# Kernel tuning notes

Measured on AMD Instinct MI355X. Metric: run time of the kernel, lower is better.

## Reference

```python
import jax, jax.numpy as jnp
import numpy as np

B, T, D = 512, 128, 512   # batch, encoder positions, input_size
H = 512                   # hidden_size
MID, BOT = 38, 38         # class counts


def setup_inputs() -> dict:
    key = jax.random.key(0)
    ks = jax.random.split(key, 12)
    s = lambda fan_in: 1.0 / np.sqrt(fan_in)
    inp = {
        "batch_H": jax.random.normal(ks[0], (B, T, D), dtype=jnp.float32),
        "mid_prev_text": jax.random.randint(ks[1], (B, 26), 0, MID, dtype=jnp.int64)
            if jax.config.jax_enable_x64 else jax.random.randint(ks[1], (B, 26), 0, MID).astype(jnp.int32),
        "bot_text": jax.random.randint(ks[2], (B, 26), 0, BOT).astype(jnp.int32),
        # AttentionCell params
        "W_i2h": jax.random.uniform(ks[3], (H, D), jnp.float32, -s(D), s(D)),
        "W_h2h": jax.random.uniform(ks[4], (H, H), jnp.float32, -s(H), s(H)),
        "b_h2h": jax.random.uniform(ks[5], (H,), jnp.float32, -s(H), s(H)),
        "W_score": jax.random.uniform(ks[6], (1, H), jnp.float32, -s(H), s(H)),
        # LSTMCell params: input dim = D + MID + BOT
        "W_ih": jax.random.uniform(ks[7], (4 * H, D + MID + BOT), jnp.float32, -s(H), s(H)),
        "W_hh": jax.random.uniform(ks[8], (4 * H, H), jnp.float32, -s(H), s(H)),
        "b_ih": jax.random.uniform(ks[9], (4 * H,), jnp.float32, -s(H), s(H)),
        "b_hh": jax.random.uniform(ks[10], (4 * H,), jnp.float32, -s(H), s(H)),
        # generator
        "W_gen": jax.random.uniform(ks[11], (MID, H), jnp.float32, -s(H), s(H)),
        "b_gen": jnp.zeros((MID,), jnp.float32),
        "batch_max_length": 25,
    }
    return inp


def reference(batch_H, mid_prev_text, bot_text, W_i2h, W_h2h, b_h2h, W_score,
              W_ih, W_hh, b_ih, b_hh, W_gen, b_gen, batch_max_length):
    num_steps = batch_max_length + 1
    bsz = batch_H.shape[0]
    hid = W_h2h.shape[0]

    # batch_H projection is step-independent: compute once. [B, T, H]
    batch_H_proj = jnp.einsum('btd,hd->bth', batch_H, W_i2h)

    # Precompute teacher-forced onehots, time-major: [num_steps, B, C]
    oh_mid = jax.nn.one_hot(mid_prev_text[:, :num_steps].T, MID, dtype=batch_H.dtype)
    oh_bot = jax.nn.one_hot(bot_text[:, :num_steps].T, BOT, dtype=batch_H.dtype)

    def step(carry, inputs):
        h, c = carry
        ohm, ohb = inputs
        # attention scores over T positions
        prev_proj = h @ W_h2h.T + b_h2h                       # [B, H]
        e = jnp.einsum('bth,oh->bto', jnp.tanh(batch_H_proj + prev_proj[:, None, :]), W_score)  # [B,T,1]
        alpha = jax.nn.softmax(e, axis=1)                     # [B, T, 1]
        context = jnp.einsum('bto,btd->bd', alpha, batch_H)   # [B, D]
        x = jnp.concatenate([context, ohm, ohb], axis=1)      # [B, D+MID+BOT]
        # LSTMCell (PyTorch gate order: i, f, g, o)
        gates = x @ W_ih.T + b_ih + h @ W_hh.T + b_hh         # [B, 4H]
        i_g, f_g, g_g, o_g = jnp.split(gates, 4, axis=1)
        i_g = jax.nn.sigmoid(i_g)
        f_g = jax.nn.sigmoid(f_g)
        g_g = jnp.tanh(g_g)
        o_g = jax.nn.sigmoid(o_g)
        c_new = f_g * c + i_g * g_g
        h_new = o_g * jnp.tanh(c_new)
        return (h_new, c_new), h_new

    h0 = jnp.zeros((bsz, hid), batch_H.dtype)
    c0 = jnp.zeros((bsz, hid), batch_H.dtype)
    (_, _), hiddens = jax.lax.scan(step, (h0, c0), (oh_mid, oh_bot))  # [S, B, H]
    output_hiddens = jnp.transpose(hiddens, (1, 0, 2))                 # [B, S, H]
    g = jnp.einsum('bsh,ch->bsc', output_hiddens, W_gen) + b_gen       # [B, S, MID]
    return g
```

## Files before the change

### kernel.cpp

```cpp
#include <hip/hip_runtime.h>
#include <hip/hip_bf16.h>
#include <hip/hip_fp16.h>
#include <cstdint>
#include <cstddef>

#define B_   512
#define T_   128
#define D_   512
#define H_   512
#define MID_ 38
#define BOT_ 38
#define S_   26
#define XL_  588

typedef unsigned short u16;
typedef __attribute__((ext_vector_type(8))) short bf16x8v;
typedef __attribute__((ext_vector_type(8))) _Float16 f16x8v;
typedef __attribute__((ext_vector_type(8))) unsigned short u16x8;
typedef __attribute__((ext_vector_type(4))) float f32x4v;

__device__ __forceinline__ u16 f2bf_rn(float f){
  unsigned u = __float_as_uint(f);
  return (u16)((u + 0x7fffu + ((u>>16)&1u)) >> 16);
}
__device__ __forceinline__ float bf2f(u16 v){ return __uint_as_float(((unsigned)v)<<16); }
__device__ __forceinline__ u16 f2h_u(float f){ return __half_as_ushort(__float2half(f)); }
__device__ __forceinline__ float h2f_u(u16 u){ return __half2float(__ushort_as_half(u)); }

__device__ __forceinline__ float fast_tanh(float x){
  return 1.0f - 2.0f*__builtin_amdgcn_rcpf(__expf(2.0f*x) + 1.0f);
}
__device__ __forceinline__ float fast_sig(float x){
  return __builtin_amdgcn_rcpf(1.0f + __expf(-x));
}

__device__ __forceinline__ void cvt_hilo4(const float* src, u16* hi, u16* lo){
  float4 v = *(const float4*)src;
  ushort4 h, l;
  h.x=f2bf_rn(v.x); h.y=f2bf_rn(v.y); h.z=f2bf_rn(v.z); h.w=f2bf_rn(v.w);
  l.x=f2bf_rn(v.x-bf2f(h.x)); l.y=f2bf_rn(v.y-bf2f(h.y));
  l.z=f2bf_rn(v.z-bf2f(h.z)); l.w=f2bf_rn(v.w-bf2f(h.w));
  *(ushort4*)hi = h; *(ushort4*)lo = l;
}

__global__ __launch_bounds__(256) void setup_all(
    const float* __restrict__ bH,
    const float* __restrict__ Wi2h, const float* __restrict__ Wh2h,
    const float* __restrict__ Whh,  const float* __restrict__ Wih,
    const float* __restrict__ Wgen, const float* __restrict__ bh2h,
    const float* __restrict__ bih,  const float* __restrict__ bhh,
    u16* __restrict__ bHh,
    u16* __restrict__ Wi2h_h, u16* __restrict__ Bh2_hi, u16* __restrict__ Bh2_lo,
    u16* __restrict__ Bih_hi, u16* __restrict__ Bih_lo,
    u16* __restrict__ Wg_hi,  u16* __restrict__ Wg_lo,
    float* __restrict__ WmT, float* __restrict__ WbT, float* __restrict__ bcombF,
    u16* __restrict__ hA_hi, u16* __restrict__ hA_lo, float* __restrict__ c)
{
  const int T0 = 8388608;
  const int T1 = T0+65536;
  const int T2 = T1+65536;
  const int T3 = T2+262144;
  const int T4 = T3+262144;
  const int T5 = T4+8192;
  const int T6 = T5+19456;
  const int T7 = T6+640;
  const int T8 = T7+65536;
  const int T9 = T8+65536;
  for (int i = blockIdx.x*256 + threadIdx.x; i < T9; i += gridDim.x*256){
    if (i < T0){
      int row=i>>7, c4=(i&127)*4;
      float4 v = *(const float4*)&bH[(size_t)row*512 + c4];
      ushort4 h; h.x=f2h_u(v.x); h.y=f2h_u(v.y); h.z=f2h_u(v.z); h.w=f2h_u(v.w);
      *(ushort4*)&bHh[(size_t)row*512 + c4] = h;
    } else if (i < T1){
      int j=i-T0, row=j>>7, c4=(j&127)*4;
      float4 v = *(const float4*)&Wi2h[(size_t)row*512 + c4];
      ushort4 h; h.x=f2h_u(v.x); h.y=f2h_u(v.y); h.z=f2h_u(v.z); h.w=f2h_u(v.w);
      *(ushort4*)&Wi2h_h[(size_t)row*512 + c4] = h;
    } else if (i < T2){
      int j=i-T1, row=j>>7, c4=(j&127)*4;
      cvt_hilo4(&Wh2h[(size_t)row*512+c4], &Bh2_hi[(size_t)row*512+c4], &Bh2_lo[(size_t)row*512+c4]);
    } else if (i < T3){
      int j=i-T2, row=j>>7, c4=(j&127)*4;
      cvt_hilo4(&Whh[(size_t)row*512+c4],
                &Bh2_hi[(size_t)(512+row)*512+c4], &Bh2_lo[(size_t)(512+row)*512+c4]);
    } else if (i < T4){
      int j=i-T3, row=j>>7, c4=(j&127)*4;
      cvt_hilo4(&Wih[(size_t)row*XL_+c4], &Bih_hi[(size_t)row*512+c4], &Bih_lo[(size_t)row*512+c4]);
    } else if (i < T5){
      int j=i-T4, row=j>>7, c4=(j&127)*4;
      float4 v = make_float4(0.f,0.f,0.f,0.f);
      if (row < MID_) v = *(const float4*)&Wgen[(size_t)row*512 + c4];
      ushort4 h, l;
      h.x=f2bf_rn(v.x); h.y=f2bf_rn(v.y); h.z=f2bf_rn(v.z); h.w=f2bf_rn(v.w);
      l.x=f2bf_rn(v.x-bf2f(h.x)); l.y=f2bf_rn(v.y-bf2f(h.y));
      l.z=f2bf_rn(v.z-bf2f(h.z)); l.w=f2bf_rn(v.w-bf2f(h.w));
      *(ushort4*)&Wg_hi[(size_t)row*512+c4] = h;
      *(ushort4*)&Wg_lo[(size_t)row*512+c4] = l;
    } else if (i < T6){
      int j=i-T5;
      int cc=j>>9, jq=j&511;
#pragma unroll
      for (int u=0;u<4;u++){
        int jj=jq*4+u;
        WmT[(size_t)cc*2048+jj] = Wih[(size_t)jj*XL_ + 512 + cc];
        WbT[(size_t)cc*2048+jj] = Wih[(size_t)jj*XL_ + 512 + MID_ + cc];
      }
    } else if (i < T7){
      int j=(i-T6)*4;
#pragma unroll
      for (int u=0;u<4;u++){
        int k=j+u;
        if (k < 512) bcombF[k] = bh2h[k];
        else if (k < 2560) bcombF[k] = bih[k-512] + bhh[k-512];
      }
    } else if (i < T8){
      int j=i-T7;
      ushort4 z = {0,0,0,0};
      *(ushort4*)&hA_hi[(size_t)j*4] = z;
      *(ushort4*)&hA_lo[(size_t)j*4] = z;
    } else {
      int j=i-T8;
      *(float4*)&c[(size_t)j*4] = make_float4(0.f,0.f,0.f,0.f);
    }
  }
}

__global__ __launch_bounds__(256) void gemm_proj16(
    const u16* __restrict__ Ah, const u16* __restrict__ Bh,
    u16* __restrict__ projh)
{
  extern __shared__ char smem[];
  constexpr int STR = 40;
  short* As = (short*)smem;
  short* Bs = As + 128*STR;
  const int tid=threadIdx.x;
  const int n = blockIdx.x;
  const int x = n & 7, q = n >> 3;
  const int bn = (q & 3) * 128;
  const int bm = ((q >> 2)*8 + x) * 128;
  const int w=tid>>6, lane=tid&63, wr=w>>1, wc=w&1;

  f32x4v acc[4][4];
#pragma unroll
  for (int i=0;i<4;i++)
#pragma unroll
    for (int j=0;j<4;j++) acc[i][j] = (f32x4v){0.f,0.f,0.f,0.f};

  u16x8 ra[2], rb[2];
  auto load = [&](int it){
    const int kk = it<<5;
#pragma unroll
    for (int L=0; L<2; L++){
      int t=L*256+tid, row=t>>2, c=(t&3)*8;
      ra[L] = *(const u16x8*)&Ah[(size_t)(bm+row)*512 + kk + c];
      rb[L] = *(const u16x8*)&Bh[(size_t)(bn+row)*512 + kk + c];
    }
  };
  load(0);

  for (int it=0; it<16; ++it){
    __syncthreads();
#pragma unroll
    for (int L=0; L<2; L++){
      int t=L*256+tid, row=t>>2, c=(t&3)*8;
      *(u16x8*)&As[row*STR+c] = ra[L];
      *(u16x8*)&Bs[row*STR+c] = rb[L];
    }
    if (it+1 < 16) load(it+1);
    __syncthreads();
    const int koff = (lane>>4)*8, mrow = lane&15;
#pragma unroll
    for (int i=0;i<4;i++)
#pragma unroll
      for (int j=0;j<4;j++){
        f16x8v af = *(const f16x8v*)&As[(wr*64+i*16+mrow)*STR + koff];
        f16x8v bf = *(const f16x8v*)&Bs[(wc*64+j*16+mrow)*STR + koff];
        acc[i][j] = __builtin_amdgcn_mfma_f32_16x16x32_f16(af, bf, acc[i][j], 0,0,0);
      }
  }

  const int r0 = (lane>>4)*4, cn = lane&15;
  __syncthreads();
  u16* Ts = (u16*)smem;
#pragma unroll
  for (int i=0;i<4;i++)
#pragma unroll
    for (int j=0;j<4;j++)
#pragma unroll
      for (int r=0;r<4;r++)
        Ts[(wr*64+i*16+r0+r)*128 + wc*64+j*16+cn] = f2h_u(acc[i][j][r]);
  __syncthreads();
#pragma unroll
  for (int q2=0;q2<8;q2++){
    int idx = q2*256 + tid;
    int row = idx>>4, c8 = (idx&15)*8;
    *(float4*)&projh[(size_t)(bm+row)*512 + bn + c8] = *(const float4*)&Ts[row*128 + c8];
  }
}

template<int BM,int BN,int MODE>
__global__ __launch_bounds__(256) void gemm_bf(
    const u16* __restrict__ Ah, const u16* __restrict__ Al, int lda,
    const u16* __restrict__ Bh, const u16* __restrict__ Bl, int ldb,
    float* __restrict__ Cout, int ldc,
    const float* __restrict__ bias2, int npass, int kSteps)
{
  extern __shared__ char smem[];
  constexpr int STR = 40;
  short* As = (short*)smem;
  short* Bs = As + BM*STR;
  const int tid=threadIdx.x, bm=blockIdx.y*BM, bn=blockIdx.x*BN;
  const int w=tid>>6, lane=tid&63, wr=w>>1, wc=w&1;
  constexpr int WM=BM/2, WN=BN/2, FM=WM/16, FN=WN/16;
  constexpr int LA=BM/64, LB=BN/64;
  const int nIter = npass*kSteps;

  f32x4v acc[FM][FN];
#pragma unroll
  for (int i=0;i<FM;i++)
#pragma unroll
    for (int j=0;j<FN;j++) acc[i][j] = (f32x4v){0.f,0.f,0.f,0.f};

  u16x8 ra[LA], rb[LB];
  auto load = [&](int it){
    const int pass = it/kSteps, kk = (it%kSteps)<<5;
    const u16* Ap = (pass==2)?Al:Ah;
    const u16* Bp = (pass==1)?Bl:Bh;
#pragma unroll
    for (int L=0; L<LA; L++){
      int t=L*256+tid, row=t>>2, c=(t&3)*8;
      ra[L] = *(const u16x8*)&Ap[(size_t)(bm+row)*lda + kk + c];
    }
#pragma unroll
    for (int L=0; L<LB; L++){
      int t=L*256+tid, row=t>>2, c=(t&3)*8;
      rb[L] = *(const u16x8*)&Bp[(size_t)(bn+row)*ldb + kk + c];
    }
  };
  load(0);

  for (int it=0; it<nIter; ++it){
    __syncthreads();
#pragma unroll
    for (int L=0; L<LA; L++){ int t=L*256+tid; *(u16x8*)&As[(t>>2)*STR+(t&3)*8] = ra[L]; }
#pragma unroll
    for (int L=0; L<LB; L++){ int t=L*256+tid; *(u16x8*)&Bs[(t>>2)*STR+(t&3)*8] = rb[L]; }
    if (it+1 < nIter) load(it+1);
    __syncthreads();
    const int koff = (lane>>4)*8, mrow = lane&15;
#pragma unroll
    for (int i=0;i<FM;i++)
#pragma unroll
      for (int j=0;j<FN;j++){
        bf16x8v af = *(const bf16x8v*)&As[(wr*WM+i*16+mrow)*STR + koff];
        bf16x8v bf = *(const bf16x8v*)&Bs[(wc*WN+j*16+mrow)*STR + koff];
        acc[i][j] = __builtin_amdgcn_mfma_f32_16x16x32_bf16(af, bf, acc[i][j], 0,0,0);
      }
  }

  const int r0 = (lane>>4)*4, cn = lane&15;
  if constexpr (MODE==2){
#pragma unroll
    for (int i=0;i<FM;i++)
#pragma unroll
      for (int j=0;j<FN;j++)
#pragma unroll
        for (int r=0;r<4;r++){
          int m = bm + wr*WM + i*16 + r0 + r;
          int n2 = bn + wc*WN + j*16 + cn;
          if (n2 < MID_){
            int s = m >> 9, b = m & 511;
            Cout[((size_t)b*S_ + s)*MID_ + n2] = acc[i][j][r] + bias2[n2];
          }
        }
  } else {
#pragma unroll
    for (int i=0;i<FM;i++)
#pragma unroll
      for (int j=0;j<FN;j++)
#pragma unroll
        for (int r=0;r<4;r++){
          int row = bm + wr*WM + i*16 + r0 + r;
          int col = bn + wc*WN + j*16 + cn;
          float v = acc[i][j][r];
          if (bias2) v += bias2[col];
          Cout[(size_t)row*ldc + col] = v;
        }
  }
}

__global__ __launch_bounds__(1024) void attn_kernel(
    const u16* __restrict__ projh, const float* __restrict__ combo,
    const float* __restrict__ Wscore, const u16* __restrict__ bHh,
    u16* __restrict__ ctx_hi, u16* __restrict__ ctx_lo)
{
  __shared__ float s_e[T_];
  __shared__ float s_red[32];
  __shared__ float s_part[16][D_];
  const int tid=threadIdx.x, b=blockIdx.x, wave=tid>>6, lane=tid&63;

  float pv[8], wv[8];
  {
    const float* pprow = combo + (size_t)b*2560;
    float4 p0=*(const float4*)&pprow[lane*8], p1=*(const float4*)&pprow[lane*8+4];
    float4 w0=*(const float4*)&Wscore[lane*8], w1=*(const float4*)&Wscore[lane*8+4];
    pv[0]=p0.x;pv[1]=p0.y;pv[2]=p0.z;pv[3]=p0.w;pv[4]=p1.x;pv[5]=p1.y;pv[6]=p1.z;pv[7]=p1.w;
    wv[0]=w0.x;wv[1]=w0.y;wv[2]=w0.z;wv[3]=w0.w;wv[4]=w1.x;wv[5]=w1.y;wv[6]=w1.z;wv[7]=w1.w;
  }
  {
    const u16* base = projh + (size_t)b*T_*H_ + lane*8;
    u16x8 cur = *(const u16x8*)(base + (size_t)wave*H_);
    for (int t=wave; t<T_; t+=16){
      u16x8 nxt;
      if (t+16 < T_) nxt = *(const u16x8*)(base + (size_t)(t+16)*H_);
      float acc = 0.f;
#pragma unroll
      for (int j=0;j<8;j++) acc += wv[j]*fast_tanh(h2f_u(cur[j]) + pv[j]);
#pragma unroll
      for (int o=32;o>0;o>>=1) acc += __shfl_down(acc,o);
      if (lane==0) s_e[t] = acc;
      cur = nxt;
    }
  }
  __syncthreads();
  float v = (tid < T_) ? s_e[tid] : -INFINITY;
  float m = v;
#pragma unroll
  for (int o=32;o>0;o>>=1) m = fmaxf(m, __shfl_down(m,o));
  if (tid < T_ && lane==0) s_red[wave] = m;
  __syncthreads();
  m = fmaxf(s_red[0], s_red[1]);
  float p = (tid < T_) ? __expf(v - m) : 0.f;
  float sum = p;
#pragma unroll
  for (int o=32;o>0;o>>=1) sum += __shfl_down(sum,o);
  if (tid < T_ && lane==0) s_red[16+wave] = sum;
  __syncthreads();
  float denom = s_red[16] + s_red[17];
  if (tid < T_) s_e[tid] = p/denom;
  __syncthreads();

  const int d0 = lane*8;
  float a[8] = {0,0,0,0,0,0,0,0};
  {
    const u16* base = bHh + (size_t)b*T_*D_ + d0;
    u16x8 cur = *(const u16x8*)(base + (size_t)(wave*8)*D_);
    for (int t=wave*8; t<wave*8+8; ++t){
      u16x8 nxt;
      if (t+1 < wave*8+8) nxt = *(const u16x8*)(base + (size_t)(t+1)*D_);
      const float al = s_e[t];
#pragma unroll
      for (int j=0;j<8;j++) a[j] += al*h2f_u(cur[j]);
      cur = nxt;
    }
  }
  *(float4*)&s_part[wave][d0]   = make_float4(a[0],a[1],a[2],a[3]);
  *(float4*)&s_part[wave][d0+4] = make_float4(a[4],a[5],a[6],a[7]);
  __syncthreads();
  if (tid < D_){
    float vv = s_part[0][tid];
#pragma unroll
    for (int q=1;q<16;q++) vv += s_part[q][tid];
    u16 hh=f2bf_rn(vv), ll=f2bf_rn(vv-bf2f(hh));
    ctx_hi[(size_t)b*512 + tid] = hh;
    ctx_lo[(size_t)b*512 + tid] = ll;
  }
}

__global__ __launch_bounds__(256) void gates_lstm(
    const u16* __restrict__ Ah, const u16* __restrict__ Al,
    const u16* __restrict__ Bh, const u16* __restrict__ Bl,
    const float* __restrict__ combo,
    const float* __restrict__ WmT, const float* __restrict__ WbT,
    const int* __restrict__ midtok, const int* __restrict__ bottok,
    float* __restrict__ c,
    u16* __restrict__ hA_hi, u16* __restrict__ hA_lo,
    u16* __restrict__ hid_hi, u16* __restrict__ hid_lo, int s)
{
  constexpr int STR = 72;
  __shared__ short Bs[64*STR];
  const int tid=threadIdx.x, lane=tid&63, w=tid>>6;
  const int j0 = blockIdx.x*16, bm = blockIdx.y*64;
  const int mrow=lane&15, koff=(lane>>4)*8;
  const int arow = bm + w*16 + mrow;
  const int srow = tid>>2, scc=(tid&3)*8;
  const int sbrow = (srow>>4)*512 + j0 + (srow&15);

  f32x4v acc[4];
#pragma unroll
  for (int f=0;f<4;f++) acc[f] = (f32x4v){0.f,0.f,0.f,0.f};

  u16x8 sb0, sb1;
  bf16x8v a0[2], a1[2];
  auto loadB = [&](int it){
    const int pass = it>>3, kk=(it&7)<<6;
    const u16* Bp = (pass==1)?Bl:Bh;
    sb0 = *(const u16x8*)&Bp[(size_t)sbrow*512 + kk + scc];
    sb1 = *(const u16x8*)&Bp[(size_t)sbrow*512 + kk + scc + 32];
  };
  auto loadA0 = [&](int it){
    const int pass = it>>3, kk=(it&7)<<6;
    const u16* Ap = (pass==2)?Al:Ah;
    a0[0] = *(const bf16x8v*)&Ap[(size_t)arow*512 + kk + koff];
    a0[1] = *(const bf16x8v*)&Ap[(size_t)arow*512 + kk + koff + 32];
  };
  auto loadA1 = [&](int it){
    const int pass = it>>3, kk=(it&7)<<6;
    const u16* Ap = (pass==2)?Al:Ah;
    a1[0] = *(const bf16x8v*)&Ap[(size_t)arow*512 + kk + koff];
    a1[1] = *(const bf16x8v*)&Ap[(size_t)arow*512 + kk + koff + 32];
  };

  loadB(0); loadA0(0);
  for (int it=0; it<24; it+=2){
    __syncthreads();
    *(u16x8*)&Bs[srow*STR+scc]    = sb0;
    *(u16x8*)&Bs[srow*STR+scc+32] = sb1;
    if (it+1 < 24){ loadB(it+1); loadA1(it+1); }
    __syncthreads();
#pragma unroll
    for (int f=0;f<4;f++){
      bf16x8v b0 = *(const bf16x8v*)&Bs[(f*16+mrow)*STR + koff];
      bf16x8v b1 = *(const bf16x8v*)&Bs[(f*16+mrow)*STR + koff + 32];
      acc[f] = __builtin_amdgcn_mfma_f32_16x16x32_bf16(a0[0], b0, acc[f], 0,0,0);
      acc[f] = __builtin_amdgcn_mfma_f32_16x16x32_bf16(a0[1], b1, acc[f], 0,0,0);
    }
    if (it+1 >= 24) break;
    __syncthreads();
    *(u16x8*)&Bs[srow*STR+scc]    = sb0;
    *(u16x8*)&Bs[srow*STR+scc+32] = sb1;
    if (it+2 < 24){ loadB(it+2); loadA0(it+2); }
    __syncthreads();
#pragma unroll
    for (int f=0;f<4;f++){
      bf16x8v b0 = *(const bf16x8v*)&Bs[(f*16+mrow)*STR + koff];
      bf16x8v b1 = *(const bf16x8v*)&Bs[(f*16+mrow)*STR + koff + 32];
      acc[f] = __builtin_amdgcn_mfma_f32_16x16x32_bf16(a1[0], b0, acc[f], 0,0,0);
      acc[f] = __builtin_amdgcn_mfma_f32_16x16x32_bf16(a1[1], b1, acc[f], 0,0,0);
    }
  }

  const int r0=(lane>>4)*4, jj=lane&15, j=j0+jj;
#pragma unroll
  for (int r=0;r<4;r++){
    const int b = bm + w*16 + r0 + r;
    const int mt = midtok[b*26 + s];
    const int bt = bottok[b*26 + s];
    const float* wm = WmT + (size_t)mt*2048;
    const float* wb = WbT + (size_t)bt*2048;
    const float* cb = combo + (size_t)b*2560 + 512;
    float ig = acc[0][r] + cb[j       ] + wm[j       ] + wb[j       ];
    float fg = acc[1][r] + cb[512 + j ] + wm[512 + j ] + wb[512 + j ];
    float gg = acc[2][r] + cb[1024 + j] + wm[1024 + j] + wb[1024 + j];
    float og = acc[3][r] + cb[1536 + j] + wm[1536 + j] + wb[1536 + j];
    ig = fast_sig(ig);
    fg = fast_sig(fg);
    gg = fast_tanh(gg);
    og = fast_sig(og);
    const size_t ci = (size_t)b*512 + j;
    const float cn = fg*c[ci] + ig*gg;
    const float hn = og*fast_tanh(cn);
    c[ci] = cn;
    u16 hh = f2bf_rn(hn), hl = f2bf_rn(hn - bf2f(hh));
    hA_hi[ci] = hh;
    hA_lo[ci] = hl;
    hid_hi[((size_t)s*512 + b)*512 + j] = hh;
    hid_lo[((size_t)s*512 + b)*512 + j] = hl;
  }
}

extern "C" void kernel_launch(void* const* d_in, const int* in_sizes, int n_in,
                              void* d_out, int out_size, void* d_ws, size_t ws_size,
                              hipStream_t stream) {
  const float* bH   = (const float*)d_in[0];
  const int*   midt = (const int*)  d_in[1];
  const int*   bott = (const int*)  d_in[2];
  const float* Wi2h = (const float*)d_in[3];
  const float* Wh2h = (const float*)d_in[4];
  const float* bh2h = (const float*)d_in[5];
  const float* Wsc  = (const float*)d_in[6];
  const float* Wih  = (const float*)d_in[7];
  const float* Whh  = (const float*)d_in[8];
  const float* bih  = (const float*)d_in[9];
  const float* bhh  = (const float*)d_in[10];
  const float* Wgen = (const float*)d_in[11];
  const float* bgen = (const float*)d_in[12];
  float* out = (float*)d_out;

  char* wp = (char*)d_ws;
  u16* projh   = (u16*)wp; wp += (size_t)B_*T_*H_*2;
  u16* bHh     = (u16*)wp; wp += (size_t)B_*T_*D_*2;
  u16* Bh2_hi  = (u16*)wp; wp += (size_t)2560*512*2;
  u16* Bh2_lo  = (u16*)wp; wp += (size_t)2560*512*2;
  u16* Bih_hi  = (u16*)wp; wp += (size_t)2048*512*2;
  u16* Bih_lo  = (u16*)wp; wp += (size_t)2048*512*2;
  u16* Wi2h_h  = (u16*)wp; wp += (size_t)512*512*2;
  u16* Wg_hi   = (u16*)wp; wp += (size_t)64*512*2;
  u16* Wg_lo   = (u16*)wp; wp += (size_t)64*512*2;
  u16* ctx_hi  = (u16*)wp; wp += (size_t)B_*512*2;
  u16* ctx_lo  = (u16*)wp; wp += (size_t)B_*512*2;
  u16* hA_hi   = (u16*)wp; wp += (size_t)B_*512*2;
  u16* hA_lo   = (u16*)wp; wp += (size_t)B_*512*2;
  u16* hid_hi  = (u16*)wp; wp += (size_t)S_*B_*H_*2;
  u16* hid_lo  = (u16*)wp; wp += (size_t)S_*B_*H_*2;
  float* combo = (float*)wp; wp += (size_t)B_*2560*4;
  float* c     = (float*)wp; wp += (size_t)B_*H_*4;
  float* bcombF= (float*)wp; wp += (size_t)2560*4;
  float* WmT   = (float*)wp; wp += (size_t)MID_*2048*4;
  float* WbT   = (float*)wp; wp += (size_t)BOT_*2048*4;
  if ((size_t)(wp - (char*)d_ws) > ws_size) return;

  setup_all<<<4096, 256, 0, stream>>>(
      bH, Wi2h, Wh2h, Whh, Wih, Wgen, bh2h, bih, bhh,
      bHh, Wi2h_h, Bh2_hi, Bh2_lo, Bih_hi, Bih_lo, Wg_hi, Wg_lo,
      WmT, WbT, bcombF, hA_hi, hA_lo, c);

  gemm_proj16<<<2048, 256, 32768, stream>>>(bHh, Wi2h_h, projh);

  for (int s=0; s<S_; ++s){
    gemm_bf<64,64,0><<<dim3(40,8), 256, 10240, stream>>>(
        hA_hi, hA_lo, 512, Bh2_hi, Bh2_lo, 512,
        combo, 2560, bcombF, 3, 16);
    attn_kernel<<<B_, 1024, 0, stream>>>(
        projh, combo, Wsc, bHh, ctx_hi, ctx_lo);
    gates_lstm<<<dim3(32,8), 256, 0, stream>>>(
        ctx_hi, ctx_lo, Bih_hi, Bih_lo, combo, WmT, WbT,
        midt, bott, c, hA_hi, hA_lo,
        hid_hi, hid_lo, s);
  }

  gemm_bf<64,64,2><<<dim3(1,208), 256, 10240, stream>>>(
      hid_hi, hid_lo, 512, Wg_hi, Wg_lo, 512,
      out, 0, bgen, 3, 16);
}
```

Before: 1.655 ms.

## Use direct global-to-LDS loads in GEMMs and streamline attention softmax

Both GEMM kernels now use global_load_lds to copy tiles straight into shared memory. This replaces the register-staged double-buffer prefetch and the padded stride of 40 with an unpadded stride of 32, and the shared-memory launch sizes shrink to match. The attention kernel prefetches the first context rows before the score loop and does the softmax in one wavefront with xor shuffles, which removes two block barriers. In exchange, loads no longer overlap compute across K iterations, and the unpadded LDS layout may cause bank conflicts on the MFMA fragment reads.

Result: slower. 1.817 ms (+9.8%).

```diff
diff --git a/kernel.cpp b/kernel.cpp
--- a/kernel.cpp
+++ b/kernel.cpp
@@ -32,6 +32,12 @@
 }
 __device__ __forceinline__ float fast_sig(float x){
   return __builtin_amdgcn_rcpf(1.0f + __expf(-x));
+}
+
+typedef __attribute__((address_space(1))) const unsigned gu32;
+typedef __attribute__((address_space(3))) unsigned lu32;
+__device__ __forceinline__ void gload16(const void* g, void* l){
+  __builtin_amdgcn_global_load_lds((gu32*)g, (lu32*)l, 16, 0, 0);
 }
 
 __device__ __forceinline__ void cvt_hilo4(const float* src, u16* hi, u16* lo){
@@ -131,9 +137,8 @@
     u16* __restrict__ projh)
 {
   extern __shared__ char smem[];
-  constexpr int STR = 40;
   short* As = (short*)smem;
-  short* Bs = As + 128*STR;
+  short* Bs = As + 128*32;
   const int tid=threadIdx.x;
   const int n = blockIdx.x;
   const int x = n & 7, q = n >> 3;
@@ -147,41 +152,28 @@
 #pragma unroll
     for (int j=0;j<4;j++) acc[i][j] = (f32x4v){0.f,0.f,0.f,0.f};
 
-  u16x8 ra[2], rb[2];
-  auto load = [&](int it){
+  for (int it=0; it<16; ++it){
     const int kk = it<<5;
 #pragma unroll
     for (int L=0; L<2; L++){
       int t=L*256+tid, row=t>>2, c=(t&3)*8;
-      ra[L] = *(const u16x8*)&Ah[(size_t)(bm+row)*512 + kk + c];
-      rb[L] = *(const u16x8*)&Bh[(size_t)(bn+row)*512 + kk + c];
-    }
-  };
-  load(0);
-
-  for (int it=0; it<16; ++it){
-    __syncthreads();
-#pragma unroll
-    for (int L=0; L<2; L++){
-      int t=L*256+tid, row=t>>2, c=(t&3)*8;
-      *(u16x8*)&As[row*STR+c] = ra[L];
-      *(u16x8*)&Bs[row*STR+c] = rb[L];
-    }
-    if (it+1 < 16) load(it+1);
+      gload16(&Ah[(size_t)(bm+row)*512 + kk + c], &As[t*8]);
+      gload16(&Bh[(size_t)(bn+row)*512 + kk + c], &Bs[t*8]);
+    }
     __syncthreads();
     const int koff = (lane>>4)*8, mrow = lane&15;
 #pragma unroll
     for (int i=0;i<4;i++)
 #pragma unroll
       for (int j=0;j<4;j++){
-        f16x8v af = *(const f16x8v*)&As[(wr*64+i*16+mrow)*STR + koff];
-        f16x8v bf = *(const f16x8v*)&Bs[(wc*64+j*16+mrow)*STR + koff];
+        f16x8v af = *(const f16x8v*)&As[(wr*64+i*16+mrow)*32 + koff];
+        f16x8v bf = *(const f16x8v*)&Bs[(wc*64+j*16+mrow)*32 + koff];
         acc[i][j] = __builtin_amdgcn_mfma_f32_16x16x32_f16(af, bf, acc[i][j], 0,0,0);
       }
+    __syncthreads();
   }
 
   const int r0 = (lane>>4)*4, cn = lane&15;
-  __syncthreads();
   u16* Ts = (u16*)smem;
 #pragma unroll
   for (int i=0;i<4;i++)
@@ -207,9 +199,8 @@
     const float* __restrict__ bias2, int npass, int kSteps)
 {
   extern __shared__ char smem[];
-  constexpr int STR = 40;
   short* As = (short*)smem;
-  short* Bs = As + BM*STR;
+  short* Bs = As + BM*32;
   const int tid=threadIdx.x, bm=blockIdx.y*BM, bn=blockIdx.x*BN;
   const int w=tid>>6, lane=tid&63, wr=w>>1, wc=w&1;
   constexpr int WM=BM/2, WN=BN/2, FM=WM/16, FN=WN/16;
@@ -222,41 +213,31 @@
 #pragma unroll
     for (int j=0;j<FN;j++) acc[i][j] = (f32x4v){0.f,0.f,0.f,0.f};
 
-  u16x8 ra[LA], rb[LB];
-  auto load = [&](int it){
+  for (int it=0; it<nIter; ++it){
     const int pass = it/kSteps, kk = (it%kSteps)<<5;
     const u16* Ap = (pass==2)?Al:Ah;
     const u16* Bp = (pass==1)?Bl:Bh;
 #pragma unroll
     for (int L=0; L<LA; L++){
       int t=L*256+tid, row=t>>2, c=(t&3)*8;
-      ra[L] = *(const u16x8*)&Ap[(size_t)(bm+row)*lda + kk + c];
+      gload16(&Ap[(size_t)(bm+row)*lda + kk + c], &As[t*8]);
     }
 #pragma unroll
     for (int L=0; L<LB; L++){
       int t=L*256+tid, row=t>>2, c=(t&3)*8;
-      rb[L] = *(const u16x8*)&Bp[(size_t)(bn+row)*ldb + kk + c];
-    }
-  };
-  load(0);
-
-  for (int it=0; it<nIter; ++it){
-    __syncthreads();
-#pragma unroll
-    for (int L=0; L<LA; L++){ int t=L*256+tid; *(u16x8*)&As[(t>>2)*STR+(t&3)*8] = ra[L]; }
-#pragma unroll
-    for (int L=0; L<LB; L++){ int t=L*256+tid; *(u16x8*)&Bs[(t>>2)*STR+(t&3)*8] = rb[L]; }
-    if (it+1 < nIter) load(it+1);
+      gload16(&Bp[(size_t)(bn+row)*ldb + kk + c], &Bs[t*8]);
+    }
     __syncthreads();
     const int koff = (lane>>4)*8, mrow = lane&15;
 #pragma unroll
     for (int i=0;i<FM;i++)
 #pragma unroll
       for (int j=0;j<FN;j++){
-        bf16x8v af = *(const bf16x8v*)&As[(wr*WM+i*16+mrow)*STR + koff];
-        bf16x8v bf = *(const bf16x8v*)&Bs[(wc*WN+j*16+mrow)*STR + koff];
+        bf16x8v af = *(const bf16x8v*)&As[(wr*WM+i*16+mrow)*32 + koff];
+        bf16x8v bf = *(const bf16x8v*)&Bs[(wc*WN+j*16+mrow)*32 + koff];
         acc[i][j] = __builtin_amdgcn_mfma_f32_16x16x32_bf16(af, bf, acc[i][j], 0,0,0);
       }
+    __syncthreads();
   }
 
   const int r0 = (lane>>4)*4, cn = lane&15;
@@ -296,9 +277,10 @@
     u16* __restrict__ ctx_hi, u16* __restrict__ ctx_lo)
 {
   __shared__ float s_e[T_];
-  __shared__ float s_red[32];
   __shared__ float s_part[16][D_];
   const int tid=threadIdx.x, b=blockIdx.x, wave=tid>>6, lane=tid&63;
+  const int d0 = lane*8;
+  const u16* cbase = bHh + (size_t)b*T_*D_ + d0;
 
   float pv[8], wv[8];
   {
@@ -308,6 +290,10 @@
     pv[0]=p0.x;pv[1]=p0.y;pv[2]=p0.z;pv[3]=p0.w;pv[4]=p1.x;pv[5]=p1.y;pv[6]=p1.z;pv[7]=p1.w;
     wv[0]=w0.x;wv[1]=w0.y;wv[2]=w0.z;wv[3]=w0.w;wv[4]=w1.x;wv[5]=w1.y;wv[6]=w1.z;wv[7]=w1.w;
   }
+  u16x8 pf[4];
+#pragma unroll
+  for (int r=0;r<4;r++) pf[r] = *(const u16x8*)(cbase + (size_t)(wave*8+r)*D_);
+
   {
     const u16* base = projh + (size_t)b*T_*H_ + lane*8;
     u16x8 cur = *(const u16x8*)(base + (size_t)wave*H_);
@@ -324,36 +310,36 @@
     }
   }
   __syncthreads();
-  float v = (tid < T_) ? s_e[tid] : -INFINITY;
-  float m = v;
-#pragma unroll
-  for (int o=32;o>0;o>>=1) m = fmaxf(m, __shfl_down(m,o));
-  if (tid < T_ && lane==0) s_red[wave] = m;
+  if (wave==0){
+    float v0 = s_e[lane], v1 = s_e[lane+64];
+    float mm = fmaxf(v0, v1);
+#pragma unroll
+    for (int o=32;o>0;o>>=1) mm = fmaxf(mm, __shfl_xor(mm,o));
+    float p0 = __expf(v0-mm), p1 = __expf(v1-mm);
+    float ss = p0 + p1;
+#pragma unroll
+    for (int o=32;o>0;o>>=1) ss += __shfl_xor(ss,o);
+    const float inv = __builtin_amdgcn_rcpf(ss);
+    s_e[lane]    = p0*inv;
+    s_e[lane+64] = p1*inv;
+  }
   __syncthreads();
-  m = fmaxf(s_red[0], s_red[1]);
-  float p = (tid < T_) ? __expf(v - m) : 0.f;
-  float sum = p;
-#pragma unroll
-  for (int o=32;o>0;o>>=1) sum += __shfl_down(sum,o);
-  if (tid < T_ && lane==0) s_red[16+wave] = sum;
-  __syncthreads();
-  float denom = s_red[16] + s_red[17];
-  if (tid < T_) s_e[tid] = p/denom;
-  __syncthreads();
-
-  const int d0 = lane*8;
+
   float a[8] = {0,0,0,0,0,0,0,0};
-  {
-    const u16* base = bHh + (size_t)b*T_*D_ + d0;
-    u16x8 cur = *(const u16x8*)(base + (size_t)(wave*8)*D_);
-    for (int t=wave*8; t<wave*8+8; ++t){
-      u16x8 nxt;
-      if (t+1 < wave*8+8) nxt = *(const u16x8*)(base + (size_t)(t+1)*D_);
-      const float al = s_e[t];
-#pragma unroll
-      for (int j=0;j<8;j++) a[j] += al*h2f_u(cur[j]);
-      cur = nxt;
-    }
+  u16x8 cur = *(const u16x8*)(cbase + (size_t)(wave*8+4)*D_);
+#pragma unroll
+  for (int r=0;r<4;r++){
+    const float al = s_e[wave*8+r];
+#pragma unroll
+    for (int j=0;j<8;j++) a[j] += al*h2f_u(pf[r][j]);
+  }
+  for (int t=wave*8+4; t<wave*8+8; ++t){
+    u16x8 nxt;
+    if (t+1 < wave*8+8) nxt = *(const u16x8*)(cbase + (size_t)(t+1)*D_);
+    const float al = s_e[t];
+#pragma unroll
+    for (int j=0;j<8;j++) a[j] += al*h2f_u(cur[j]);
+    cur = nxt;
   }
   *(float4*)&s_part[wave][d0]   = make_float4(a[0],a[1],a[2],a[3]);
   *(float4*)&s_part[wave][d0+4] = make_float4(a[4],a[5],a[6],a[7]);
@@ -519,7 +505,7 @@
   gemm_proj16<<<2048, 256, 32768, stream>>>(bHh, Wi2h_h, projh);
 
   for (int s=0; s<S_; ++s){
-    gemm_bf<64,64,0><<<dim3(40,8), 256, 10240, stream>>>(
+    gemm_bf<64,64,0><<<dim3(40,8), 256, 8192, stream>>>(
         hA_hi, hA_lo, 512, Bh2_hi, Bh2_lo, 512,
         combo, 2560, bcombF, 3, 16);
     attn_kernel<<<B_, 1024, 0, stream>>>(
@@ -530,7 +516,7 @@
         hid_hi, hid_lo, s);
   }
 
-  gemm_bf<64,64,2><<<dim3(1,208), 256, 10240, stream>>>(
+  gemm_bf<64,64,2><<<dim3(1,208), 256, 8192, stream>>>(
       hid_hi, hid_lo, 512, Wg_hi, Wg_lo, 512,
       out, 0, bgen, 3, 16);
 }
```
